# Optimization experiments

Hardware: AMD Instinct MI355X
Metric: run time of the kernel (lower is better)

## Reference

```python
import jax, jax.numpy as jnp
import numpy as np

D_MODEL = 14
N_HEADS = 2
SINK_TEMP = 0.1
SINK_ITERS = 20
EPS = 1e-10


def setup_inputs() -> dict:
    key = jax.random.key(0)
    ks = jax.random.split(key, 12)
    b, n, d = 64, 1024, D_MODEL
    s = 1.0 / np.sqrt(d)
    return {
        "x": jax.random.normal(ks[0], (b, n, d), dtype=jnp.float32),
        "certainty": jax.random.uniform(ks[1], (b, n), dtype=jnp.float32),
        "permutation": jax.random.randint(ks[2], (b, n), 0, n).astype(jnp.int64),
        "Wq": jax.random.normal(ks[3], (d, d), dtype=jnp.float32) * s,
        "bq": jnp.zeros((d,), dtype=jnp.float32),
        "Wk": jax.random.normal(ks[4], (d, d), dtype=jnp.float32) * s,
        "bk": jnp.zeros((d,), dtype=jnp.float32),
        "Wv": jax.random.normal(ks[5], (d, d), dtype=jnp.float32) * s,
        "bv": jnp.zeros((d,), dtype=jnp.float32),
        "Wo": jax.random.normal(ks[6], (d, d), dtype=jnp.float32) * s,
        "bo": jnp.zeros((d,), dtype=jnp.float32),
    }


def _split_heads(t, b, n):
    # (b, n, d) -> (b, H, n, hd)
    return t.reshape(b, n, N_HEADS, D_MODEL // N_HEADS).transpose(0, 2, 1, 3)


def reference(x, certainty, permutation, Wq, bq, Wk, bk, Wv, bv, Wo, bo):
    b, n, d = x.shape
    hd = d // N_HEADS
    Q = _split_heads(x @ Wq.T + bq, b, n)
    K = _split_heads(x @ Wk.T + bk, b, n)
    V = _split_heads(x @ Wv.T + bv, b, n)
    scores = jnp.einsum("bhqd,bhkd->bhqk", Q, K) / jnp.sqrt(jnp.float32(hd))
    attn = jax.nn.softmax(scores, axis=-1)  # dropout is identity at eval
    out = jnp.einsum("bhqk,bhkd->bhqd", attn, V)
    out = out.transpose(0, 2, 1, 3).reshape(b, n, d)
    out = out @ Wo.T + bo

    avg_attn = attn.mean(axis=1)  # (b, n, n)
    entropy = -jnp.sum(avg_attn * jnp.log(avg_attn + EPS), axis=-1)  # (b, n)
    max_entropy = jnp.log(jnp.float32(n))
    cert_update = jax.nn.sigmoid(max_entropy - entropy)
    new_certainty = jnp.maximum(certainty, cert_update)

    logits = jnp.log(avg_attn + EPS)
    P = jnp.exp(logits / SINK_TEMP)

    def body(_, P):
        P = P / (P.sum(axis=-1, keepdims=True) + EPS)
        P = P / (P.sum(axis=-2, keepdims=True) + EPS)
        return P

    P = jax.lax.fori_loop(0, SINK_ITERS, body, P)
    new_perm = jnp.argmax(P, axis=-1)  # (b, n)
    new_permutation = jnp.take_along_axis(permutation, new_perm, axis=1)
    return out, new_certainty, new_permutation
```

## Files before the change

### kernel.cpp

```cpp
#include <hip/hip_runtime.h>

#define EPSF    1e-10f
#define MAXENT  6.93147180559945286f
#define SCALEF  0.37796447300922720f

__device__ __forceinline__ float wave_sum(float v) {
#pragma unroll
  for (int off = 32; off > 0; off >>= 1) v += __shfl_xor(v, off);
  return v;
}
__device__ __forceinline__ void wave_sum2(float& a, float& b) {
#pragma unroll
  for (int off = 32; off > 0; off >>= 1) {
    a += __shfl_xor(a, off);
    b += __shfl_xor(b, off);
  }
}
__device__ __forceinline__ void fma4(float a, float4 b, float4& c) {
  c.x = fmaf(a, b.x, c.x); c.y = fmaf(a, b.y, c.y);
  c.z = fmaf(a, b.z, c.z); c.w = fmaf(a, b.w, c.w);
}
__device__ __forceinline__ float dot4(float4 a, float4 b, float acc) {
  acc = fmaf(a.x, b.x, acc); acc = fmaf(a.y, b.y, acc);
  acc = fmaf(a.z, b.z, acc); acc = fmaf(a.w, b.w, acc);
  return acc;
}
__device__ __forceinline__ float exp4sum(float4 s) {
  return __expf(s.x) + __expf(s.y) + __expf(s.z) + __expf(s.w);
}
__device__ __forceinline__ float p0e(float s1, float s2, float E1, float E2) {
  float p = fmaf(E1, __expf(s1), fmaf(E2, __expf(s2), EPSF));
  float p2 = p * p, p4 = p2 * p2, p5 = p4 * p;
  return p5 * p5;
}

__global__ __launch_bounds__(256) void qkv_kernel(
    const float* __restrict__ x,
    const float* __restrict__ Wq, const float* __restrict__ bq,
    const float* __restrict__ Wk, const float* __restrict__ bk,
    const float* __restrict__ Wv, const float* __restrict__ bv,
    float* __restrict__ Qt, float* __restrict__ Kt, float* __restrict__ Vt,
    float* __restrict__ R, float* __restrict__ CA, float* __restrict__ CB) {
  int row = blockIdx.x * 256 + threadIdx.x;
  int b = row >> 10, i = row & 1023;
  float xv[14];
#pragma unroll
  for (int k = 0; k < 14; k++) xv[k] = x[row * 14 + k];
#pragma unroll
  for (int d = 0; d < 14; d++) {
    float q = bq[d], kk = bk[d], vv = bv[d];
#pragma unroll
    for (int k = 0; k < 14; k++) {
      q  = fmaf(xv[k], Wq[d * 14 + k], q);
      kk = fmaf(xv[k], Wk[d * 14 + k], kk);
      vv = fmaf(xv[k], Wv[d * 14 + k], vv);
    }
    int o = b * 14336 + d * 1024 + i;
    Qt[o] = q * SCALEF;
    Kt[o] = kk; Vt[o] = vv;
  }
  R[row] = 1.0f;
  CA[row] = 1.0f;
  CB[row] = 1.0f;
}

__global__ __launch_bounds__(512) void attn_kernel(
    const float* __restrict__ Qt, const float* __restrict__ Kt, const float* __restrict__ Vt,
    const float* __restrict__ cert_in,
    float* __restrict__ E1o, float* __restrict__ E2o,
    float* __restrict__ attn_o, float* __restrict__ cert_out) {
  __shared__ float4 Kl[3584];
  int b = blockIdx.x >> 6;
  int rg = blockIdx.x & 63;
  int tid = threadIdx.x;
  const float4* Ktb = (const float4*)(Kt + b * 14336);
  for (int idx = tid; idx < 3584; idx += 512) Kl[idx] = Ktb[idx];
  __syncthreads();

  int wave = tid >> 6, lane = tid & 63;
  int i0 = rg * 16 + wave * 2;
  float q0[14], q1[14];
#pragma unroll
  for (int d = 0; d < 14; d++) {
    q0[d] = Qt[b * 14336 + d * 1024 + i0];
    q1[d] = Qt[b * 14336 + d * 1024 + i0 + 1];
  }

  float L10 = 0.f, L20 = 0.f, L11 = 0.f, L21 = 0.f;
#pragma unroll
  for (int t = 0; t < 4; t++) {
    int g = t * 64 + lane;
    float4 kv[7];
#pragma unroll
    for (int d = 0; d < 7; d++) kv[d] = Kl[d * 256 + g];
    float4 sa = {0,0,0,0}, sb = {0,0,0,0};
#pragma unroll
    for (int d = 0; d < 7; d++) { fma4(q0[d], kv[d], sa); fma4(q1[d], kv[d], sb); }
    L10 += exp4sum(sa); L11 += exp4sum(sb);
#pragma unroll
    for (int d = 0; d < 7; d++) kv[d] = Kl[(d + 7) * 256 + g];
    sa = make_float4(0,0,0,0); sb = make_float4(0,0,0,0);
#pragma unroll
    for (int d = 0; d < 7; d++) { fma4(q0[d + 7], kv[d], sa); fma4(q1[d + 7], kv[d], sb); }
    L20 += exp4sum(sa); L21 += exp4sum(sb);
  }
  L10 = wave_sum(L10); L20 = wave_sum(L20);
  L11 = wave_sum(L11); L21 = wave_sum(L21);
  float i10 = 1.0f / L10, i20 = 1.0f / L20, i11 = 1.0f / L11, i21 = 1.0f / L21;

  float acc0[14], acc1[14];
#pragma unroll
  for (int d = 0; d < 14; d++) { acc0[d] = 0.f; acc1[d] = 0.f; }
  float ent0 = 0.f, ent1 = 0.f;
  const float4* Vtb = (const float4*)(Vt + b * 14336);
#pragma unroll
  for (int t = 0; t < 4; t++) {
    int g = t * 64 + lane;
    float4 kv[7];
#pragma unroll
    for (int d = 0; d < 7; d++) kv[d] = Kl[d * 256 + g];
    float4 sa = {0,0,0,0}, sb = {0,0,0,0};
#pragma unroll
    for (int d = 0; d < 7; d++) { fma4(q0[d], kv[d], sa); fma4(q1[d], kv[d], sb); }
    float4 e10 = make_float4(__expf(sa.x), __expf(sa.y), __expf(sa.z), __expf(sa.w));
    float4 e11 = make_float4(__expf(sb.x), __expf(sb.y), __expf(sb.z), __expf(sb.w));
#pragma unroll
    for (int d = 0; d < 7; d++) kv[d] = Kl[(d + 7) * 256 + g];
    sa = make_float4(0,0,0,0); sb = make_float4(0,0,0,0);
#pragma unroll
    for (int d = 0; d < 7; d++) { fma4(q0[d + 7], kv[d], sa); fma4(q1[d + 7], kv[d], sb); }
    float4 e20 = make_float4(__expf(sa.x), __expf(sa.y), __expf(sa.z), __expf(sa.w));
    float4 e21 = make_float4(__expf(sb.x), __expf(sb.y), __expf(sb.z), __expf(sb.w));
#pragma unroll
    for (int d = 0; d < 7; d++) {
      float4 vv = Vtb[d * 256 + g];
      acc0[d] += e10.x * vv.x + e10.y * vv.y + e10.z * vv.z + e10.w * vv.w;
      acc1[d] += e11.x * vv.x + e11.y * vv.y + e11.z * vv.z + e11.w * vv.w;
    }
#pragma unroll
    for (int d = 7; d < 14; d++) {
      float4 vv = Vtb[d * 256 + g];
      acc0[d] += e20.x * vv.x + e20.y * vv.y + e20.z * vv.z + e20.w * vv.w;
      acc1[d] += e21.x * vv.x + e21.y * vv.y + e21.z * vv.z + e21.w * vv.w;
    }
    float a;
    a = 0.5f * (e10.x * i10 + e20.x * i20); ent0 -= a * __logf(a + EPSF);
    a = 0.5f * (e10.y * i10 + e20.y * i20); ent0 -= a * __logf(a + EPSF);
    a = 0.5f * (e10.z * i10 + e20.z * i20); ent0 -= a * __logf(a + EPSF);
    a = 0.5f * (e10.w * i10 + e20.w * i20); ent0 -= a * __logf(a + EPSF);
    a = 0.5f * (e11.x * i11 + e21.x * i21); ent1 -= a * __logf(a + EPSF);
    a = 0.5f * (e11.y * i11 + e21.y * i21); ent1 -= a * __logf(a + EPSF);
    a = 0.5f * (e11.z * i11 + e21.z * i21); ent1 -= a * __logf(a + EPSF);
    a = 0.5f * (e11.w * i11 + e21.w * i21); ent1 -= a * __logf(a + EPSF);
  }
  ent0 = wave_sum(ent0); ent1 = wave_sum(ent1);
#pragma unroll
  for (int d = 0; d < 14; d++) { acc0[d] = wave_sum(acc0[d]); acc1[d] = wave_sum(acc1[d]); }

  if (lane == 0) {
    int row0 = b * 1024 + i0;
    E1o[row0] = 0.5f * i10;  E2o[row0] = 0.5f * i20;
    E1o[row0 + 1] = 0.5f * i11; E2o[row0 + 1] = 0.5f * i21;
#pragma unroll
    for (int d = 0; d < 14; d++) {
      attn_o[row0 * 14 + d] = acc0[d] * (d < 7 ? i10 : i20);
      attn_o[(row0 + 1) * 14 + d] = acc1[d] * (d < 7 ? i11 : i21);
    }
    cert_out[row0] = fmaxf(cert_in[row0], 1.0f / (1.0f + __expf(ent0 - MAXENT)));
    cert_out[row0 + 1] = fmaxf(cert_in[row0 + 1], 1.0f / (1.0f + __expf(ent1 - MAXENT)));
  }
}

__global__ __launch_bounds__(256) void proj_kernel(
    const float* __restrict__ attn_o, const float* __restrict__ Wo,
    const float* __restrict__ bo, float* __restrict__ out) {
  int idx = blockIdx.x * 256 + threadIdx.x;
  if (idx >= 917504) return;
  int row = idx / 14, d = idx - row * 14;
  float s = bo[d];
  const float* ar = attn_o + row * 14;
  const float* wr = Wo + d * 14;
#pragma unroll
  for (int k = 0; k < 14; k++) s = fmaf(ar[k], wr[k], s);
  out[idx] = s;
}


__global__ __launch_bounds__(512) void p0sink1_kernel(
    const float* __restrict__ Qt, const float* __restrict__ Kt,
    const float* __restrict__ E1, const float* __restrict__ E2,
    float* __restrict__ P0, float* __restrict__ R,
    float* __restrict__ vpart, int b0, int G) {
  __shared__ float4 Kl[3584];
  int gb = blockIdx.x >> 5, blk = blockIdx.x & 31;
  int b = b0 + gb;
  int tid = threadIdx.x;
  const float4* Ktb = (const float4*)(Kt + b * 14336);
  for (int idx = tid; idx < 3584; idx += 512) Kl[idx] = Ktb[idx];
  __syncthreads();

  int wave = tid >> 6, lane = tid & 63;
  int i0 = blk * 32 + wave * 4;
  float q[4][14], e1r[4], e2r[4], u[4];
#pragma unroll
  for (int rr = 0; rr < 4; rr++) {
#pragma unroll
    for (int d = 0; d < 14; d++) q[rr][d] = Qt[b * 14336 + d * 1024 + i0 + rr];
    e1r[rr] = E1[b * 1024 + i0 + rr];
    e2r[rr] = E2[b * 1024 + i0 + rr];
    u[rr] = 0.f;
  }
  float4* P0f4 = (float4*)P0;
#pragma unroll
  for (int t = 0; t < 4; t++) {
    int g = t * 64 + lane;
    float4 kv[14];
#pragma unroll
    for (int d = 0; d < 14; d++) kv[d] = Kl[d * 256 + g];
#pragma unroll
    for (int rr = 0; rr < 4; rr++) {
      float4 s1 = {0,0,0,0}, s2 = {0,0,0,0};
#pragma unroll
      for (int d = 0; d < 7; d++)  fma4(q[rr][d], kv[d], s1);
#pragma unroll
      for (int d = 7; d < 14; d++) fma4(q[rr][d], kv[d], s2);
      float4 pv;
      pv.x = p0e(s1.x, s2.x, e1r[rr], e2r[rr]);
      pv.y = p0e(s1.y, s2.y, e1r[rr], e2r[rr]);
      pv.z = p0e(s1.z, s2.z, e1r[rr], e2r[rr]);
      pv.w = p0e(s1.w, s2.w, e1r[rr], e2r[rr]);
      P0f4[(size_t)(gb * 1024 + i0 + rr) * 256 + g] = pv;
      u[rr] += pv.x; u[rr] += pv.y; u[rr] += pv.z; u[rr] += pv.w;
    }
  }
  wave_sum2(u[0], u[1]); wave_sum2(u[2], u[3]);
  float rv[4];
#pragma unroll
  for (int rr = 0; rr < 4; rr++) {
    float r0 = 1.0f;
    rv[rr] = fminf(r0 / fmaf(r0, u[rr], EPSF), 1e37f);
  }
  if (lane == 0) {
#pragma unroll
    for (int rr = 0; rr < 4; rr++) R[b * 1024 + i0 + rr] = rv[rr];
  }
  int l0 = lane, l1 = 64 + lane, l2 = 128 + lane, l3 = 192 + lane;
  float4 v0 = {0,0,0,0}, v1 = {0,0,0,0}, v2 = {0,0,0,0}, v3 = {0,0,0,0};
  const float4* base = P0f4 + (size_t)(gb * 1024 + i0) * 256;
#pragma unroll
  for (int rr = 0; rr < 4; rr++) {
    const float4* row = base + rr * 256;
    float4 a0 = row[l0], a1 = row[l1], a2 = row[l2], a3 = row[l3];
    fma4(rv[rr], a0, v0); fma4(rv[rr], a1, v1); fma4(rv[rr], a2, v2); fma4(rv[rr], a3, v3);
  }
  __syncthreads();
  float* vbuf = (float*)Kl;
  float4* vb4 = (float4*)vbuf;
  vb4[wave * 256 + l0] = v0; vb4[wave * 256 + l1] = v1;
  vb4[wave * 256 + l2] = v2; vb4[wave * 256 + l3] = v3;
  __syncthreads();
  for (int col = tid; col < 1024; col += 512) {
    float v = 0.f;
#pragma unroll
    for (int w = 0; w < 8; w++) v += vbuf[w * 1024 + col];
    vpart[(size_t)(blk * G + gb) * 1024 + col] = v;
  }
}

#define SINK_LOGS 4
#define SINK_S    16
__global__ __launch_bounds__(512) void sink_fused(
    const float* __restrict__ P0, const float* __restrict__ Cin,
    float* __restrict__ Cout, float* __restrict__ R,
    const float* __restrict__ vprev, float* __restrict__ vcur,
    int b0, int G, int Sprev) {
  __shared__ float Cl[1024];
  __shared__ float vbuf[8192];
  int tid = threadIdx.x;
  int gb = blockIdx.x >> SINK_LOGS, slice = blockIdx.x & (SINK_S - 1);
  int b = b0 + gb;

  if (tid < 256) {
    float4 cv = ((const float4*)(Cin + b * 1024))[tid];
    const float4* vp = (const float4*)vprev + (size_t)gb * 256 + tid;
    float4 v = {0, 0, 0, 0};
#pragma unroll 4
    for (int s = 0; s < Sprev; s++) {
      float4 t = vp[(size_t)s * G * 256];
      v.x += t.x; v.y += t.y; v.z += t.z; v.w += t.w;
    }
    cv.x = fminf(cv.x / fmaf(cv.x, v.x, EPSF), 1e37f);
    cv.y = fminf(cv.y / fmaf(cv.y, v.y, EPSF), 1e37f);
    cv.z = fminf(cv.z / fmaf(cv.z, v.z, EPSF), 1e37f);
    cv.w = fminf(cv.w / fmaf(cv.w, v.w, EPSF), 1e37f);
    if (slice == 0) ((float4*)(Cout + b * 1024))[tid] = cv;
    ((float4*)Cl)[tid] = cv;
  }
  __syncthreads();

  int wave = tid >> 6, lane = tid & 63;
  int i0 = slice * 64 + wave * 8;
  int rbase = b * 1024 + i0;
  int l0 = lane, l1 = 64 + lane, l2 = 128 + lane, l3 = 192 + lane;
  const float4* Cl4 = (const float4*)Cl;
  float4 c0 = Cl4[l0], c1 = Cl4[l1], c2 = Cl4[l2], c3 = Cl4[l3];
  float4 v0 = {0,0,0,0}, v1 = {0,0,0,0}, v2 = {0,0,0,0}, v3 = {0,0,0,0};
  const float4* base = (const float4*)P0 + (size_t)(gb * 1024 + i0) * 256;

  float rreg[8];
#pragma unroll
  for (int r = 0; r < 8; r++) rreg[r] = R[rbase + r];

  float4 a0 = base[l0], a1 = base[l1], a2 = base[l2], a3 = base[l3];
  float4 b0f = base[256 + l0], b1f = base[256 + l1], b2f = base[256 + l2], b3f = base[256 + l3];

#pragma unroll
  for (int r = 0; r < 8; r += 2) {
    float4 na0, na1, na2, na3, nb0, nb1, nb2, nb3;
    if (r + 2 < 8) {
      const float4* nxt = base + (r + 2) * 256;
      na0 = nxt[l0]; na1 = nxt[l1]; na2 = nxt[l2]; na3 = nxt[l3];
      nb0 = nxt[256 + l0]; nb1 = nxt[256 + l1]; nb2 = nxt[256 + l2]; nb3 = nxt[256 + l3];
    }
    float ua = dot4(a3, c3, dot4(a2, c2, dot4(a1, c1, dot4(a0, c0, 0.f))));
    float ub = dot4(b3f, c3, dot4(b2f, c2, dot4(b1f, c1, dot4(b0f, c0, 0.f))));
    wave_sum2(ua, ub);
    float rva = rreg[r], rvb = rreg[r + 1];
    rva = fminf(rva / fmaf(rva, ua, EPSF), 1e37f);
    rvb = fminf(rvb / fmaf(rvb, ub, EPSF), 1e37f);
    if (lane == 0) { R[rbase + r] = rva; R[rbase + r + 1] = rvb; }
    fma4(rva, a0, v0); fma4(rva, a1, v1); fma4(rva, a2, v2); fma4(rva, a3, v3);
    fma4(rvb, b0f, v0); fma4(rvb, b1f, v1); fma4(rvb, b2f, v2); fma4(rvb, b3f, v3);
    if (r + 2 < 8) {
      a0 = na0; a1 = na1; a2 = na2; a3 = na3;
      b0f = nb0; b1f = nb1; b2f = nb2; b3f = nb3;
    }
  }
  float4* vb4 = (float4*)vbuf;
  vb4[wave * 256 + l0] = v0; vb4[wave * 256 + l1] = v1;
  vb4[wave * 256 + l2] = v2; vb4[wave * 256 + l3] = v3;
  __syncthreads();
  for (int col = tid; col < 1024; col += 512) {
    float v = 0.f;
#pragma unroll
    for (int w = 0; w < 8; w++) v += vbuf[w * 1024 + col];
    vcur[(size_t)(slice * G + gb) * 1024 + col] = v;
  }
}

__global__ __launch_bounds__(256) void cfinal_kernel(
    const float* __restrict__ Cin, float* __restrict__ Cfin,
    const float* __restrict__ vprev, int b0, int G) {
  int idx = blockIdx.x * 256 + threadIdx.x;
  int gb = idx >> 10, col = idx & 1023;
  const float* vp = vprev + gb * 1024 + col;
  float v = 0.f;
#pragma unroll
  for (int s = 0; s < SINK_S; s++) v += vp[(size_t)s * G * 1024];
  int o = (b0 + gb) * 1024 + col;
  float cv = Cin[o];
  Cfin[o] = fminf(cv / fmaf(cv, v, EPSF), 1e37f);
}

__global__ __launch_bounds__(512) void argmaxP_kernel(
    const float* __restrict__ P0, const float* __restrict__ Cg,
    const int* __restrict__ perm, float* __restrict__ perm_out, int b0) {
  int gb = blockIdx.x >> 7, rg = blockIdx.x & 127;
  int b = b0 + gb;
  int tid = threadIdx.x;
  int wave = tid >> 6, lane = tid & 63;
  int i = rg * 8 + wave;
  const float4* Cb = (const float4*)(Cg + b * 1024);
  const float4* Prow = (const float4*)P0 + (size_t)(gb * 1024 + i) * 256;

  float best = -1.0f;
  int bj = 0;
#pragma unroll
  for (int t = 0; t < 4; t++) {
    int g = t * 64 + lane;
    float4 pv = Prow[g], cv = Cb[g];
    float val;
    val = pv.x * cv.x; if (val > best) { best = val; bj = 4 * g + 0; }
    val = pv.y * cv.y; if (val > best) { best = val; bj = 4 * g + 1; }
    val = pv.z * cv.z; if (val > best) { best = val; bj = 4 * g + 2; }
    val = pv.w * cv.w; if (val > best) { best = val; bj = 4 * g + 3; }
  }
#pragma unroll
  for (int off = 32; off > 0; off >>= 1) {
    float ob = __shfl_xor(best, off);
    int oj = __shfl_xor(bj, off);
    if (ob > best || (ob == best && oj < bj)) { best = ob; bj = oj; }
  }
  if (lane == 0) perm_out[b * 1024 + i] = (float)perm[b * 1024 + bj];
}


__global__ __launch_bounds__(512) void sinkA_kernel(
    const float* __restrict__ Qt, const float* __restrict__ Kt,
    const float* __restrict__ E1, const float* __restrict__ E2,
    const float* __restrict__ C, float* __restrict__ R) {
  __shared__ float4 Kl[3584];
  int b = blockIdx.x >> 5, blk = blockIdx.x & 31;
  int tid = threadIdx.x;
  const float4* Ktb = (const float4*)(Kt + b * 14336);
  for (int idx = tid; idx < 3584; idx += 512) Kl[idx] = Ktb[idx];
  __syncthreads();
  int wave = tid >> 6, lane = tid & 63;
  int i0 = blk * 32 + wave * 4;
  float q[4][14], e1r[4], e2r[4], u[4];
#pragma unroll
  for (int rr = 0; rr < 4; rr++) {
#pragma unroll
    for (int d = 0; d < 14; d++) q[rr][d] = Qt[b * 14336 + d * 1024 + i0 + rr];
    e1r[rr] = E1[b * 1024 + i0 + rr];
    e2r[rr] = E2[b * 1024 + i0 + rr];
    u[rr] = 0.f;
  }
  const float4* Cb = (const float4*)(C + b * 1024);
#pragma unroll
  for (int t = 0; t < 4; t++) {
    int g = t * 64 + lane;
    float4 kv[14];
#pragma unroll
    for (int d = 0; d < 14; d++) kv[d] = Kl[d * 256 + g];
    float4 cv = Cb[g];
#pragma unroll
    for (int rr = 0; rr < 4; rr++) {
      float4 s1 = {0,0,0,0}, s2 = {0,0,0,0};
#pragma unroll
      for (int d = 0; d < 7; d++)  fma4(q[rr][d], kv[d], s1);
#pragma unroll
      for (int d = 7; d < 14; d++) fma4(q[rr][d], kv[d], s2);
      u[rr] += p0e(s1.x, s2.x, e1r[rr], e2r[rr]) * cv.x;
      u[rr] += p0e(s1.y, s2.y, e1r[rr], e2r[rr]) * cv.y;
      u[rr] += p0e(s1.z, s2.z, e1r[rr], e2r[rr]) * cv.z;
      u[rr] += p0e(s1.w, s2.w, e1r[rr], e2r[rr]) * cv.w;
    }
  }
#pragma unroll
  for (int rr = 0; rr < 4; rr++) u[rr] = wave_sum(u[rr]);
  if (lane == 0) {
#pragma unroll
    for (int rr = 0; rr < 4; rr++) {
      int o = b * 1024 + i0 + rr;
      float rv = R[o];
      R[o] = fminf(rv / fmaf(rv, u[rr], EPSF), 1e37f);
    }
  }
}

__global__ __launch_bounds__(512) void sinkB_kernel(
    const float* __restrict__ Qt, const float* __restrict__ Kt,
    const float* __restrict__ E1, const float* __restrict__ E2,
    const float* __restrict__ R, float* __restrict__ C) {
  __shared__ float4 Ql[3584];
  int b = blockIdx.x >> 5, blk = blockIdx.x & 31;
  int tid = threadIdx.x;
  const float4* Qtb = (const float4*)(Qt + b * 14336);
  for (int idx = tid; idx < 3584; idx += 512) Ql[idx] = Qtb[idx];
  __syncthreads();
  int wave = tid >> 6, lane = tid & 63;
  int j0 = blk * 32 + wave * 4;
  float kk[4][14], v[4];
#pragma unroll
  for (int rr = 0; rr < 4; rr++) {
#pragma unroll
    for (int d = 0; d < 14; d++) kk[rr][d] = Kt[b * 14336 + d * 1024 + j0 + rr];
    v[rr] = 0.f;
  }
  const float4* E1b = (const float4*)(E1 + b * 1024);
  const float4* E2b = (const float4*)(E2 + b * 1024);
  const float4* Rb  = (const float4*)(R + b * 1024);
#pragma unroll
  for (int t = 0; t < 4; t++) {
    int g = t * 64 + lane;
    float4 qv[14];
#pragma unroll
    for (int d = 0; d < 14; d++) qv[d] = Ql[d * 256 + g];
    float4 e1v = E1b[g], e2v = E2b[g], rv = Rb[g];
#pragma unroll
    for (int rr = 0; rr < 4; rr++) {
      float4 s1 = {0,0,0,0}, s2 = {0,0,0,0};
#pragma unroll
      for (int d = 0; d < 7; d++)  fma4(kk[rr][d], qv[d], s1);
#pragma unroll
      for (int d = 7; d < 14; d++) fma4(kk[rr][d], qv[d], s2);
      v[rr] += p0e(s1.x, s2.x, e1v.x, e2v.x) * rv.x;
      v[rr] += p0e(s1.y, s2.y, e1v.y, e2v.y) * rv.y;
      v[rr] += p0e(s1.z, s2.z, e1v.z, e2v.z) * rv.z;
      v[rr] += p0e(s1.w, s2.w, e1v.w, e2v.w) * rv.w;
    }
  }
#pragma unroll
  for (int rr = 0; rr < 4; rr++) v[rr] = wave_sum(v[rr]);
  if (lane == 0) {
#pragma unroll
    for (int rr = 0; rr < 4; rr++) {
      int o = b * 1024 + j0 + rr;
      float cv = C[o];
      C[o] = fminf(cv / fmaf(cv, v[rr], EPSF), 1e37f);
    }
  }
}

__global__ __launch_bounds__(512) void argmax_kernel(
    const float* __restrict__ Qt, const float* __restrict__ Kt,
    const float* __restrict__ E1, const float* __restrict__ E2,
    const float* __restrict__ C, const int* __restrict__ perm,
    float* __restrict__ perm_out) {
  __shared__ float4 Kl[3584];
  int b = blockIdx.x >> 7, rg = blockIdx.x & 127;
  int tid = threadIdx.x;
  const float4* Ktb = (const float4*)(Kt + b * 14336);
  for (int idx = tid; idx < 3584; idx += 512) Kl[idx] = Ktb[idx];
  __syncthreads();
  int wave = tid >> 6, lane = tid & 63;
  int i = rg * 8 + wave;
  int row = b * 1024 + i;
  float q[14];
#pragma unroll
  for (int d = 0; d < 14; d++) q[d] = Qt[b * 14336 + d * 1024 + i];
  float e1r = E1[row], e2r = E2[row];
  const float4* Cb = (const float4*)(C + b * 1024);
  float best = -1.0f;
  int bj = 0;
#pragma unroll
  for (int t = 0; t < 4; t++) {
    int g = t * 64 + lane;
    float4 kv[14];
#pragma unroll
    for (int d = 0; d < 14; d++) kv[d] = Kl[d * 256 + g];
    float4 cv = Cb[g];
    float4 s1 = {0,0,0,0}, s2 = {0,0,0,0};
#pragma unroll
    for (int d = 0; d < 7; d++)  fma4(q[d], kv[d], s1);
#pragma unroll
    for (int d = 7; d < 14; d++) fma4(q[d], kv[d], s2);
    float val;
    val = p0e(s1.x, s2.x, e1r, e2r) * cv.x; if (val > best) { best = val; bj = 4 * g + 0; }
    val = p0e(s1.y, s2.y, e1r, e2r) * cv.y; if (val > best) { best = val; bj = 4 * g + 1; }
    val = p0e(s1.z, s2.z, e1r, e2r) * cv.z; if (val > best) { best = val; bj = 4 * g + 2; }
    val = p0e(s1.w, s2.w, e1r, e2r) * cv.w; if (val > best) { best = val; bj = 4 * g + 3; }
  }
#pragma unroll
  for (int off = 32; off > 0; off >>= 1) {
    float ob = __shfl_xor(best, off);
    int oj = __shfl_xor(bj, off);
    if (ob > best || (ob == best && oj < bj)) { best = ob; bj = oj; }
  }
  if (lane == 0) perm_out[row] = (float)perm[b * 1024 + bj];
}

extern "C" void kernel_launch(void* const* d_in, const int* in_sizes, int n_in,
                              void* d_out, int out_size, void* d_ws, size_t ws_size,
                              hipStream_t stream) {
  const float* x    = (const float*)d_in[0];
  const float* cert = (const float*)d_in[1];
  const int*   perm = (const int*)d_in[2];
  const float* Wq = (const float*)d_in[3];
  const float* bq = (const float*)d_in[4];
  const float* Wk = (const float*)d_in[5];
  const float* bk = (const float*)d_in[6];
  const float* Wv = (const float*)d_in[7];
  const float* bv = (const float*)d_in[8];
  const float* Wo = (const float*)d_in[9];
  const float* bo = (const float*)d_in[10];

  float* out      = (float*)d_out;
  float* cert_out = out + 917504;
  float* perm_out = out + 983040;

  float* ws = (float*)d_ws;
  float* Qt = ws;
  float* Kt = Qt + 917504;
  float* Vt = Kt + 917504;
  float* E1 = Vt + 917504;
  float* E2 = E1 + 65536;
  float* R  = E2 + 65536;
  float* CA = R + 65536;
  float* CB = CA + 65536;
  float* attn_o = CB + 65536;
  float* vpp0   = attn_o + 917504;

  size_t base_f = 3997696u;
  size_t avail_f = (ws_size / 4 > base_f) ? (ws_size / 4 - base_f) : 0;
  size_t perG = 2u * 32 * 1024 + 1048576u;
  int G = 0;
  if (avail_f >= 64 * perG) G = 64;
  else if (avail_f >= 32 * perG) G = 32;
  else if (avail_f >= 16 * perG) G = 16;

  float* Cbuf[2] = {CA, CB};

  qkv_kernel<<<256, 256, 0, stream>>>(x, Wq, bq, Wk, bk, Wv, bv, Qt, Kt, Vt, R, CA, CB);
  attn_kernel<<<4096, 512, 0, stream>>>(Qt, Kt, Vt, cert, E1, E2, attn_o, cert_out);
  proj_kernel<<<3584, 256, 0, stream>>>(attn_o, Wo, bo, out);

  if (G >= 16) {
    float* vpp[2] = {vpp0, vpp0 + (size_t)32 * G * 1024};
    float* P0 = vpp0 + (size_t)2 * 32 * G * 1024;
    for (int b0 = 0; b0 < 64; b0 += G) {
      p0sink1_kernel<<<G * 32, 512, 0, stream>>>(Qt, Kt, E1, E2, P0, R, vpp[1], b0, G);
      for (int it = 2; it <= 20; it++) {
        const float* vprev = vpp[(it - 1) & 1];
        float* vcur = vpp[it & 1];
        const float* Cin = Cbuf[it & 1];
        float* Cout = Cbuf[(it + 1) & 1];
        int Sprev = (it == 2) ? 32 : 16;
        sink_fused<<<G * SINK_S, 512, 0, stream>>>(P0, Cin, Cout, R, vprev, vcur, b0, G, Sprev);
      }
      cfinal_kernel<<<G * 4, 256, 0, stream>>>(Cbuf[1], Cbuf[0], vpp[0], b0, G);
      argmaxP_kernel<<<G * 128, 512, 0, stream>>>(P0, Cbuf[0], perm, perm_out, b0);
    }
  } else {
    for (int it = 0; it < 20; it++) {
      sinkA_kernel<<<2048, 512, 0, stream>>>(Qt, Kt, E1, E2, CA, R);
      sinkB_kernel<<<2048, 512, 0, stream>>>(Qt, Kt, E1, E2, R, CA);
    }
    argmax_kernel<<<8192, 512, 0, stream>>>(Qt, Kt, E1, E2, CA, perm, perm_out);
  }
}
```

Measured before the change: 1.426 ms.

## Fuse output projection into attention kernel and merge softmax passes

Removes the separate output-projection kernel and its attn_o workspace buffer by applying Wo/bo inside the attention kernel, with the weights staged in shared memory. The two passes over K are merged into one: exponentials are kept in registers, the PV accumulation runs alongside the row-sum accumulation, and normalization is applied afterwards. Blocks shrink to 256 threads with a 2-blocks-per-CU launch bound, so twice as many blocks each reload the full K tile into LDS. Register pressure rises because the exponentials are held across the loop.

```diff
diff --git a/kernel.cpp b/kernel.cpp
--- a/kernel.cpp
+++ b/kernel.cpp
@@ -25,8 +25,8 @@
   acc = fmaf(a.z, b.z, acc); acc = fmaf(a.w, b.w, acc);
   return acc;
 }
-__device__ __forceinline__ float exp4sum(float4 s) {
-  return __expf(s.x) + __expf(s.y) + __expf(s.z) + __expf(s.w);
+__device__ __forceinline__ float4 exp4(float4 s) {
+  return make_float4(__expf(s.x), __expf(s.y), __expf(s.z), __expf(s.w));
 }
 __device__ __forceinline__ float p0e(float s1, float s2, float E1, float E2) {
   float p = fmaf(E1, __expf(s1), fmaf(E2, __expf(s2), EPSF));
@@ -64,21 +64,26 @@
   CB[row] = 1.0f;
 }
 
-__global__ __launch_bounds__(512) void attn_kernel(
+__global__ __launch_bounds__(256, 2) void attn_kernel(
     const float* __restrict__ Qt, const float* __restrict__ Kt, const float* __restrict__ Vt,
     const float* __restrict__ cert_in,
+    const float* __restrict__ WoG, const float* __restrict__ boG,
     float* __restrict__ E1o, float* __restrict__ E2o,
-    float* __restrict__ attn_o, float* __restrict__ cert_out) {
+    float* __restrict__ out_, float* __restrict__ cert_out) {
   __shared__ float4 Kl[3584];
-  int b = blockIdx.x >> 6;
-  int rg = blockIdx.x & 63;
+  __shared__ float WoS[196];
+  __shared__ float boS[14];
+  int b = blockIdx.x >> 7;
+  int rg = blockIdx.x & 127;
   int tid = threadIdx.x;
   const float4* Ktb = (const float4*)(Kt + b * 14336);
-  for (int idx = tid; idx < 3584; idx += 512) Kl[idx] = Ktb[idx];
+  for (int idx = tid; idx < 3584; idx += 256) Kl[idx] = Ktb[idx];
+  if (tid < 196) WoS[tid] = WoG[tid];
+  if (tid < 14) boS[tid] = boG[tid];
   __syncthreads();
 
   int wave = tid >> 6, lane = tid & 63;
-  int i0 = rg * 16 + wave * 2;
+  int i0 = rg * 8 + wave * 2;
   float q0[14], q1[14];
 #pragma unroll
   for (int d = 0; d < 14; d++) {
@@ -86,7 +91,12 @@
     q1[d] = Qt[b * 14336 + d * 1024 + i0 + 1];
   }
 
+  float4 e10[4], e20[4], e11[4], e21[4];
   float L10 = 0.f, L20 = 0.f, L11 = 0.f, L21 = 0.f;
+  float acc0[14], acc1[14];
+#pragma unroll
+  for (int d = 0; d < 14; d++) { acc0[d] = 0.f; acc1[d] = 0.f; }
+  const float4* Vtb = (const float4*)(Vt + b * 14336);
 #pragma unroll
   for (int t = 0; t < 4; t++) {
     int g = t * 64 + lane;
@@ -96,93 +106,76 @@
     float4 sa = {0,0,0,0}, sb = {0,0,0,0};
 #pragma unroll
     for (int d = 0; d < 7; d++) { fma4(q0[d], kv[d], sa); fma4(q1[d], kv[d], sb); }
-    L10 += exp4sum(sa); L11 += exp4sum(sb);
+    e10[t] = exp4(sa); e11[t] = exp4(sb);
+    L10 += e10[t].x + e10[t].y + e10[t].z + e10[t].w;
+    L11 += e11[t].x + e11[t].y + e11[t].z + e11[t].w;
 #pragma unroll
     for (int d = 0; d < 7; d++) kv[d] = Kl[(d + 7) * 256 + g];
     sa = make_float4(0,0,0,0); sb = make_float4(0,0,0,0);
 #pragma unroll
     for (int d = 0; d < 7; d++) { fma4(q0[d + 7], kv[d], sa); fma4(q1[d + 7], kv[d], sb); }
-    L20 += exp4sum(sa); L21 += exp4sum(sb);
-  }
-  L10 = wave_sum(L10); L20 = wave_sum(L20);
-  L11 = wave_sum(L11); L21 = wave_sum(L21);
-  float i10 = 1.0f / L10, i20 = 1.0f / L20, i11 = 1.0f / L11, i21 = 1.0f / L21;
-
-  float acc0[14], acc1[14];
-#pragma unroll
-  for (int d = 0; d < 14; d++) { acc0[d] = 0.f; acc1[d] = 0.f; }
-  float ent0 = 0.f, ent1 = 0.f;
-  const float4* Vtb = (const float4*)(Vt + b * 14336);
-#pragma unroll
-  for (int t = 0; t < 4; t++) {
-    int g = t * 64 + lane;
-    float4 kv[7];
-#pragma unroll
-    for (int d = 0; d < 7; d++) kv[d] = Kl[d * 256 + g];
-    float4 sa = {0,0,0,0}, sb = {0,0,0,0};
-#pragma unroll
-    for (int d = 0; d < 7; d++) { fma4(q0[d], kv[d], sa); fma4(q1[d], kv[d], sb); }
-    float4 e10 = make_float4(__expf(sa.x), __expf(sa.y), __expf(sa.z), __expf(sa.w));
-    float4 e11 = make_float4(__expf(sb.x), __expf(sb.y), __expf(sb.z), __expf(sb.w));
-#pragma unroll
-    for (int d = 0; d < 7; d++) kv[d] = Kl[(d + 7) * 256 + g];
-    sa = make_float4(0,0,0,0); sb = make_float4(0,0,0,0);
-#pragma unroll
-    for (int d = 0; d < 7; d++) { fma4(q0[d + 7], kv[d], sa); fma4(q1[d + 7], kv[d], sb); }
-    float4 e20 = make_float4(__expf(sa.x), __expf(sa.y), __expf(sa.z), __expf(sa.w));
-    float4 e21 = make_float4(__expf(sb.x), __expf(sb.y), __expf(sb.z), __expf(sb.w));
+    e20[t] = exp4(sa); e21[t] = exp4(sb);
+    L20 += e20[t].x + e20[t].y + e20[t].z + e20[t].w;
+    L21 += e21[t].x + e21[t].y + e21[t].z + e21[t].w;
 #pragma unroll
     for (int d = 0; d < 7; d++) {
       float4 vv = Vtb[d * 256 + g];
-      acc0[d] += e10.x * vv.x + e10.y * vv.y + e10.z * vv.z + e10.w * vv.w;
-      acc1[d] += e11.x * vv.x + e11.y * vv.y + e11.z * vv.z + e11.w * vv.w;
+      acc0[d] += e10[t].x * vv.x + e10[t].y * vv.y + e10[t].z * vv.z + e10[t].w * vv.w;
+      acc1[d] += e11[t].x * vv.x + e11[t].y * vv.y + e11[t].z * vv.z + e11[t].w * vv.w;
     }
 #pragma unroll
     for (int d = 7; d < 14; d++) {
       float4 vv = Vtb[d * 256 + g];
-      acc0[d] += e20.x * vv.x + e20.y * vv.y + e20.z * vv.z + e20.w * vv.w;
-      acc1[d] += e21.x * vv.x + e21.y * vv.y + e21.z * vv.z + e21.w * vv.w;
-    }
+      acc0[d] += e20[t].x * vv.x + e20[t].y * vv.y + e20[t].z * vv.z + e20[t].w * vv.w;
+      acc1[d] += e21[t].x * vv.x + e21[t].y * vv.y + e21[t].z * vv.z + e21[t].w * vv.w;
+    }
+  }
+  wave_sum2(L10, L20); wave_sum2(L11, L21);
+  float i10 = 1.0f / L10, i20 = 1.0f / L20, i11 = 1.0f / L11, i21 = 1.0f / L21;
+
+  float ent0 = 0.f, ent1 = 0.f;
+#pragma unroll
+  for (int t = 0; t < 4; t++) {
     float a;
-    a = 0.5f * (e10.x * i10 + e20.x * i20); ent0 -= a * __logf(a + EPSF);
-    a = 0.5f * (e10.y * i10 + e20.y * i20); ent0 -= a * __logf(a + EPSF);
-    a = 0.5f * (e10.z * i10 + e20.z * i20); ent0 -= a * __logf(a + EPSF);
-    a = 0.5f * (e10.w * i10 + e20.w * i20); ent0 -= a * __logf(a + EPSF);
-    a = 0.5f * (e11.x * i11 + e21.x * i21); ent1 -= a * __logf(a + EPSF);
-    a = 0.5f * (e11.y * i11 + e21.y * i21); ent1 -= a * __logf(a + EPSF);
-    a = 0.5f * (e11.z * i11 + e21.z * i21); ent1 -= a * __logf(a + EPSF);
-    a = 0.5f * (e11.w * i11 + e21.w * i21); ent1 -= a * __logf(a + EPSF);
-  }
-  ent0 = wave_sum(ent0); ent1 = wave_sum(ent1);
-#pragma unroll
-  for (int d = 0; d < 14; d++) { acc0[d] = wave_sum(acc0[d]); acc1[d] = wave_sum(acc1[d]); }
-
+    a = 0.5f * (e10[t].x * i10 + e20[t].x * i20); ent0 -= a * __logf(a + EPSF);
+    a = 0.5f * (e10[t].y * i10 + e20[t].y * i20); ent0 -= a * __logf(a + EPSF);
+    a = 0.5f * (e10[t].z * i10 + e20[t].z * i20); ent0 -= a * __logf(a + EPSF);
+    a = 0.5f * (e10[t].w * i10 + e20[t].w * i20); ent0 -= a * __logf(a + EPSF);
+    a = 0.5f * (e11[t].x * i11 + e21[t].x * i21); ent1 -= a * __logf(a + EPSF);
+    a = 0.5f * (e11[t].y * i11 + e21[t].y * i21); ent1 -= a * __logf(a + EPSF);
+    a = 0.5f * (e11[t].z * i11 + e21[t].z * i21); ent1 -= a * __logf(a + EPSF);
+    a = 0.5f * (e11[t].w * i11 + e21[t].w * i21); ent1 -= a * __logf(a + EPSF);
+  }
+  wave_sum2(ent0, ent1);
+#pragma unroll
+  for (int d = 0; d < 14; d += 2) wave_sum2(acc0[d], acc0[d + 1]);
+#pragma unroll
+  for (int d = 0; d < 14; d += 2) wave_sum2(acc1[d], acc1[d + 1]);
+
+  int row0 = b * 1024 + i0;
   if (lane == 0) {
-    int row0 = b * 1024 + i0;
     E1o[row0] = 0.5f * i10;  E2o[row0] = 0.5f * i20;
     E1o[row0 + 1] = 0.5f * i11; E2o[row0 + 1] = 0.5f * i21;
-#pragma unroll
-    for (int d = 0; d < 14; d++) {
-      attn_o[row0 * 14 + d] = acc0[d] * (d < 7 ? i10 : i20);
-      attn_o[(row0 + 1) * 14 + d] = acc1[d] * (d < 7 ? i11 : i21);
-    }
     cert_out[row0] = fmaxf(cert_in[row0], 1.0f / (1.0f + __expf(ent0 - MAXENT)));
     cert_out[row0 + 1] = fmaxf(cert_in[row0 + 1], 1.0f / (1.0f + __expf(ent1 - MAXENT)));
   }
-}
-
-__global__ __launch_bounds__(256) void proj_kernel(
-    const float* __restrict__ attn_o, const float* __restrict__ Wo,
-    const float* __restrict__ bo, float* __restrict__ out) {
-  int idx = blockIdx.x * 256 + threadIdx.x;
-  if (idx >= 917504) return;
-  int row = idx / 14, d = idx - row * 14;
-  float s = bo[d];
-  const float* ar = attn_o + row * 14;
-  const float* wr = Wo + d * 14;
-#pragma unroll
-  for (int k = 0; k < 14; k++) s = fmaf(ar[k], wr[k], s);
-  out[idx] = s;
+  if (lane < 14) {
+    int d = lane;
+    float av0[14], av1[14];
+#pragma unroll
+    for (int k = 0; k < 14; k++) {
+      av0[k] = acc0[k] * (k < 7 ? i10 : i20);
+      av1[k] = acc1[k] * (k < 7 ? i11 : i21);
+    }
+    float s0 = boS[d], s1 = boS[d];
+#pragma unroll
+    for (int k = 0; k < 14; k++) {
+      s0 = fmaf(av0[k], WoS[d * 14 + k], s0);
+      s1 = fmaf(av1[k], WoS[d * 14 + k], s1);
+    }
+    out_[(size_t)row0 * 14 + d] = s0;
+    out_[(size_t)(row0 + 1) * 14 + d] = s1;
+  }
 }
 
 
@@ -579,10 +572,9 @@
   float* R  = E2 + 65536;
   float* CA = R + 65536;
   float* CB = CA + 65536;
-  float* attn_o = CB + 65536;
-  float* vpp0   = attn_o + 917504;
-
-  size_t base_f = 3997696u;
+  float* vpp0 = CB + 65536;
+
+  size_t base_f = 3080192u;
   size_t avail_f = (ws_size / 4 > base_f) ? (ws_size / 4 - base_f) : 0;
   size_t perG = 2u * 32 * 1024 + 1048576u;
   int G = 0;
@@ -593,8 +585,7 @@
   float* Cbuf[2] = {CA, CB};
 
   qkv_kernel<<<256, 256, 0, stream>>>(x, Wq, bq, Wk, bk, Wv, bv, Qt, Kt, Vt, R, CA, CB);
-  attn_kernel<<<4096, 512, 0, stream>>>(Qt, Kt, Vt, cert, E1, E2, attn_o, cert_out);
-  proj_kernel<<<3584, 256, 0, stream>>>(attn_o, Wo, bo, out);
+  attn_kernel<<<8192, 256, 0, stream>>>(Qt, Kt, Vt, cert, Wo, bo, E1, E2, out, cert_out);
 
   if (G >= 16) {
     float* vpp[2] = {vpp0, vpp0 + (size_t)32 * G * 1024};
```

Result: no change. 1.423 ms (median of 2 runs) (-0.2%).
